# Kernel optimization log

Hardware: AMD Instinct MI355X
Metric: run time of the kernel (lower is better)

## Reference

```python
import jax, jax.numpy as jnp
import numpy as np

SAMPLE_SIZE = 8192
K = 8
N_SPLATS = 1_000_000
EPS = 1e-12  # keeps sqrt grad finite on zero-distance (duplicate) pairs


def setup_inputs() -> dict:
    key = jax.random.key(0)
    k1, k2, k3 = jax.random.split(key, 3)
    means = jax.random.normal(k1, (N_SPLATS, 3), dtype=jnp.float32)
    sh0 = jax.random.normal(k2, (N_SPLATS, 1, 3), dtype=jnp.float32)
    idx = jax.random.randint(k3, (SAMPLE_SIZE,), 0, N_SPLATS, dtype=jnp.int64)
    return {"means": means, "sh0": sh0, "idx": idx}


def reference(means, sh0, idx):
    sh0 = sh0.squeeze(1)                    # [N, 3]
    sm = means[idx]                         # [S, 3] sampled positions
    ss = sh0[idx]                           # [S, 3] sampled colors
    # pairwise euclidean distances (torch.cdist, p=2): [S, S]
    sq = jnp.sum(sm * sm, axis=-1)
    d2 = sq[:, None] + sq[None, :] - 2.0 * (sm @ sm.T)
    dist = jnp.sqrt(jnp.maximum(d2, EPS))
    # k+1 smallest per row; drop self (column 0)
    _, knn_idx = jax.lax.top_k(-dist, K + 1)           # [S, K+1]
    knn_idx = knn_idx[:, 1:]                           # [S, K]
    neighbors_sh0 = ss[knn_idx]                        # [S, K, 3]
    neighbor_dist = jnp.take_along_axis(dist, knn_idx, axis=1)[..., None]  # [S, K, 1]
    weight = jnp.exp(-neighbor_dist)
    diff = ss[:, None, :] - neighbors_sh0              # [S, K, 3]
    return jnp.mean(weight * diff * diff)
```

## Files before the change

### kernel.cpp

```cpp
#include <hip/hip_runtime.h>
#include <float.h>
#include <math.h>

#define NSAMPLE 8192
#define KSEL 9
#define KNN 8
#define BLK 256
#define EPS_F 1e-12f

#define ROWS_PB 8
#define PAIRS 4
#define SUBS 64
#define KPT (NSAMPLE / SUBS)
#define BNDK 32
#define BATCH 4
#define SLOTS 256
#define SLOTP 257
#define IDX_MASK 0x1FFFu
#define VAL_MASK 0xFFFFE000u
#define PROW 73
#define SROW 289
#define SCALE (1.0f / (float)(NSAMPLE * KNN * 3))

__device__ __forceinline__ unsigned umn(unsigned a, unsigned b) { return a < b ? a : b; }
__device__ __forceinline__ unsigned umx(unsigned a, unsigned b) { return a > b ? a : b; }

__device__ __forceinline__ void insert9(unsigned s[KSEL], unsigned x)
{
#pragma unroll
    for (int k = 0; k < KSEL - 1; ++k)
        s[k] = umx(s[k + 1], umn(x, s[k]));
    s[KSEL - 1] = umn(x, s[KSEL - 1]);
}

__device__ __forceinline__ unsigned pack_d2(float d2, int gidx)
{
    return (__float_as_uint(fmaxf(d2, 0.0f)) & VAL_MASK) | (unsigned)gidx;
}

__global__ __launch_bounds__(256) void gather_k(
    const float* __restrict__ means, const float* __restrict__ sh0,
    const int* __restrict__ idx,
    float4* __restrict__ sm4, float4* __restrict__ ss4)
{
    int i = blockIdx.x * 256 + threadIdx.x;
    if (i >= NSAMPLE) return;
    int id = idx[i];
    const float* m = means + 3 * id;
    const float* s = sh0 + 3 * id;
    float mx = m[0], my = m[1], mz = m[2];
    sm4[i] = make_float4(mx, my, mz, fmaf(mx, mx, fmaf(my, my, mz * mz)));
    ss4[i] = make_float4(s[0], s[1], s[2], 0.0f);
}

__global__ __launch_bounds__(BLK, 4) void main_k(
    const float4* __restrict__ sm4, const float4* __restrict__ ss4,
    float* __restrict__ out)
{
    __shared__ unsigned surv[ROWS_PB * SLOTP];
    __shared__ unsigned scratch[ROWS_PB * SROW];
    __shared__ unsigned bpart[ROWS_PB * SUBS];
    __shared__ unsigned partS[ROWS_PB * PROW];
    __shared__ unsigned scnt[ROWS_PB];
    __shared__ unsigned bnd[ROWS_PB];
    __shared__ float    red[ROWS_PB];

    const int t = threadIdx.x;
    const int sub = t & (SUBS - 1);
    const int pair = t >> 6;
    const int rowA = pair, rowB = pair + PAIRS;
    if (t < ROWS_PB) scnt[t] = 0u;

    const float4 pA = sm4[blockIdx.x * ROWS_PB + rowA];
    const float4 pB = sm4[blockIdx.x * ROWS_PB + rowB];
    const float aX = -2.0f * pA.x, aY = -2.0f * pA.y, aZ = -2.0f * pA.z, aW = pA.w;
    const float bX = -2.0f * pB.x, bY = -2.0f * pB.y, bZ = -2.0f * pB.z, bW = pB.w;

    {
        unsigned pmA = 0xFFFFFFFFu, pmB = 0xFFFFFFFFu;
#pragma unroll 8
        for (int k = 0; k < BNDK; ++k) {
            float4 q = sm4[k * SUBS + sub];
            float sA = aW + q.w, sB = bW + q.w;
            float dA = fmaf(aX, q.x, fmaf(aY, q.y, fmaf(aZ, q.z, sA)));
            float dB = fmaf(bX, q.x, fmaf(bY, q.y, fmaf(bZ, q.z, sB)));
            pmA = umn(pmA, pack_d2(dA, k * SUBS + sub));
            pmB = umn(pmB, pack_d2(dB, k * SUBS + sub));
        }
        bpart[rowA * SUBS + sub] = pmA;
        bpart[rowB * SUBS + sub] = pmB;
    }
    __syncthreads();
    if (t < ROWS_PB) {
        unsigned s[KSEL];
#pragma unroll
        for (int k = 0; k < KSEL; ++k) s[k] = 0xFFFFFFFFu;
#pragma unroll
        for (int e = 0; e < SUBS; ++e) insert9(s, bpart[t * SUBS + e]);
        bnd[t] = s[0];
    }
    __syncthreads();

    const float bfA = __uint_as_float(bnd[rowA] | IDX_MASK);
    const float bfB = __uint_as_float(bnd[rowB] | IDX_MASK);

    for (int k0 = 0; k0 < KPT; k0 += BATCH) {
        float4 qr[BATCH];
#pragma unroll
        for (int u = 0; u < BATCH; ++u)
            qr[u] = sm4[(k0 + u) * SUBS + sub];
#pragma unroll
        for (int u = 0; u < BATCH; ++u) {
            float sA = aW + qr[u].w, sB = bW + qr[u].w;
            float dA = fmaf(aX, qr[u].x, fmaf(aY, qr[u].y, fmaf(aZ, qr[u].z, sA)));
            float dB = fmaf(bX, qr[u].x, fmaf(bY, qr[u].y, fmaf(bZ, qr[u].z, sB)));
            bool cA = (dA <= bfA), cB = (dB <= bfB);
            if (__any(cA || cB)) {
                int ci = (k0 + u) * SUBS + sub;
                if (cA) {
                    unsigned pos = atomicAdd(&scnt[rowA], 1u);
                    if (pos < SLOTS) surv[rowA * SLOTP + pos] = pack_d2(dA, ci);
                }
                if (cB) {
                    unsigned pos = atomicAdd(&scnt[rowB], 1u);
                    if (pos < SLOTS) surv[rowB * SLOTP + pos] = pack_d2(dB, ci);
                }
            }
        }
    }
    __syncthreads();

    {
        const int r1 = t & (ROWS_PB - 1);
        const int g  = t >> 3;
        const unsigned n = umn(scnt[r1], SLOTS);
        unsigned s[KSEL];
#pragma unroll
        for (int k = 0; k < KSEL; ++k) s[k] = 0xFFFFFFFFu;
        for (unsigned k = g; k < n; k += 32)
            insert9(s, surv[r1 * SLOTP + k]);
#pragma unroll
        for (int k = 0; k < KSEL; ++k)
            scratch[r1 * SROW + g * KSEL + k] = s[k];
    }
    __syncthreads();

    if (t < ROWS_PB * 8) {
        const int r1 = t & (ROWS_PB - 1);
        const int mg = t >> 3;
        unsigned m[KSEL];
#pragma unroll
        for (int k = 0; k < KSEL; ++k) m[k] = 0xFFFFFFFFu;
#pragma unroll
        for (int e = 0; e < 4 * KSEL; ++e)
            insert9(m, scratch[r1 * SROW + (4 * mg) * KSEL + e]);
#pragma unroll
        for (int k = 0; k < KSEL; ++k)
            partS[r1 * PROW + mg * KSEL + k] = m[k];
    }
    __syncthreads();

    if (t < ROWS_PB) {
        unsigned m[KSEL];
#pragma unroll
        for (int k = 0; k < KSEL; ++k) m[k] = 0xFFFFFFFFu;
#pragma unroll
        for (int e = 0; e < 8 * KSEL; ++e)
            insert9(m, partS[t * PROW + e]);

        const int gr = blockIdx.x * ROWS_PB + t;
        float4 pm4 = sm4[gr];
        float4 ps4 = ss4[gr];
        float acc = 0.0f;
#pragma unroll
        for (int k = 0; k < KNN; ++k) {
            int j = (int)(m[k] & IDX_MASK);
            float4 qm = sm4[j];
            float dx = pm4.x - qm.x, dy = pm4.y - qm.y, dz = pm4.z - qm.z;
            float d2 = fmaf(dx, dx, fmaf(dy, dy, dz * dz));
            float d = sqrtf(fmaxf(d2, EPS_F));
            float w = expf(-d);
            float4 qs = ss4[j];
            float ax = ps4.x - qs.x, ay = ps4.y - qs.y, az = ps4.z - qs.z;
            acc += w * (ax * ax + ay * ay + az * az);
        }
        red[t] = acc;
    }
    __syncthreads();
    if (t == 0) {
        float ssum = 0.0f;
#pragma unroll
        for (int i = 0; i < ROWS_PB; ++i) ssum += red[i];
        atomicAdd(out, ssum * SCALE);
    }
}

extern "C" void kernel_launch(void* const* d_in, const int* in_sizes, int n_in,
                              void* d_out, int out_size, void* d_ws, size_t ws_size,
                              hipStream_t stream)
{
    const float* means = (const float*)d_in[0];
    const float* sh0   = (const float*)d_in[1];
    const int*   idxp  = (const int*)d_in[2];

    float4* sm4 = (float4*)d_ws;
    float4* ss4 = sm4 + NSAMPLE;

    gather_k<<<NSAMPLE / 256, 256, 0, stream>>>(means, sh0, idxp, sm4, ss4);
    main_k<<<NSAMPLE / ROWS_PB, BLK, 0, stream>>>(sm4, ss4, (float*)d_out);
}
```

Measured before the change: 112.3 us.

## Use 512-thread blocks with 4 rows per thread and candidate-range split across waves

Doubles the block to 512 threads. Each thread now handles 4 query rows over a quarter of the candidate range instead of 2 rows over the full range, so each loaded candidate is reused across more rows. The bound-estimation pass samples 2048 candidates with a hierarchical top-9 reduction instead of 2048 over one serial 64-way merge. The ballot-gated survivor insertion is now done per row. This raises register pressure (launch bounds of 8) and adds extra synchronised reduction stages before the main scan.

After: 104.9 us. 1.07x faster.

```diff
diff --git a/kernel.cpp b/kernel.cpp
--- a/kernel.cpp
+++ b/kernel.cpp
@@ -5,17 +5,18 @@
 #define NSAMPLE 8192
 #define KSEL 9
 #define KNN 8
-#define BLK 256
+#define BLK 512
 #define EPS_F 1e-12f
 
 #define ROWS_PB 8
-#define PAIRS 4
-#define SUBS 64
-#define KPT (NSAMPLE / SUBS)
-#define BNDK 32
+#define RPT 4
+#define LANES 64
+#define KQT 32
+#define BNDI 8
 #define BATCH 4
 #define SLOTS 256
-#define SLOTP 257
+#define SLOTP 260
+#define BP 264
 #define IDX_MASK 0x1FFFu
 #define VAL_MASK 0xFFFFE000u
 #define PROW 73
@@ -53,86 +54,133 @@
     ss4[i] = make_float4(s[0], s[1], s[2], 0.0f);
 }
 
-__global__ __launch_bounds__(BLK, 4) void main_k(
+__global__ __launch_bounds__(BLK, 8) void main_k(
     const float4* __restrict__ sm4, const float4* __restrict__ ss4,
     float* __restrict__ out)
 {
     __shared__ unsigned surv[ROWS_PB * SLOTP];
     __shared__ unsigned scratch[ROWS_PB * SROW];
-    __shared__ unsigned bpart[ROWS_PB * SUBS];
+    __shared__ unsigned bpart[ROWS_PB * BP];
     __shared__ unsigned partS[ROWS_PB * PROW];
     __shared__ unsigned scnt[ROWS_PB];
     __shared__ unsigned bnd[ROWS_PB];
     __shared__ float    red[ROWS_PB];
 
     const int t = threadIdx.x;
-    const int sub = t & (SUBS - 1);
-    const int pair = t >> 6;
-    const int rowA = pair, rowB = pair + PAIRS;
+    const int lane = t & (LANES - 1);
+    const int w = t >> 6;
+    const int rpar = w & 1;
+    const int quarter = w >> 1;
     if (t < ROWS_PB) scnt[t] = 0u;
 
-    const float4 pA = sm4[blockIdx.x * ROWS_PB + rowA];
-    const float4 pB = sm4[blockIdx.x * ROWS_PB + rowB];
-    const float aX = -2.0f * pA.x, aY = -2.0f * pA.y, aZ = -2.0f * pA.z, aW = pA.w;
-    const float bX = -2.0f * pB.x, bY = -2.0f * pB.y, bZ = -2.0f * pB.z, bW = pB.w;
+    float cX[RPT], cY[RPT], cZ[RPT], cW[RPT];
+#pragma unroll
+    for (int i = 0; i < RPT; ++i) {
+        float4 p = sm4[blockIdx.x * ROWS_PB + rpar + 2 * i];
+        cX[i] = -2.0f * p.x; cY[i] = -2.0f * p.y; cZ[i] = -2.0f * p.z;
+        cW[i] = p.w;
+    }
 
     {
-        unsigned pmA = 0xFFFFFFFFu, pmB = 0xFFFFFFFFu;
-#pragma unroll 8
-        for (int k = 0; k < BNDK; ++k) {
-            float4 q = sm4[k * SUBS + sub];
-            float sA = aW + q.w, sB = bW + q.w;
-            float dA = fmaf(aX, q.x, fmaf(aY, q.y, fmaf(aZ, q.z, sA)));
-            float dB = fmaf(bX, q.x, fmaf(bY, q.y, fmaf(bZ, q.z, sB)));
-            pmA = umn(pmA, pack_d2(dA, k * SUBS + sub));
-            pmB = umn(pmB, pack_d2(dB, k * SUBS + sub));
+        unsigned pm[RPT];
+#pragma unroll
+        for (int i = 0; i < RPT; ++i) pm[i] = 0xFFFFFFFFu;
+        const int b0 = quarter * (BNDI * LANES);
+#pragma unroll
+        for (int k = 0; k < BNDI; ++k) {
+            const int ci = b0 + k * LANES + lane;
+            float4 q = sm4[ci];
+#pragma unroll
+            for (int i = 0; i < RPT; ++i) {
+                float d2 = fmaf(cX[i], q.x,
+                           fmaf(cY[i], q.y, fmaf(cZ[i], q.z, cW[i] + q.w)));
+                pm[i] = umn(pm[i], pack_d2(d2, ci));
+            }
         }
-        bpart[rowA * SUBS + sub] = pmA;
-        bpart[rowB * SUBS + sub] = pmB;
+#pragma unroll
+        for (int i = 0; i < RPT; ++i)
+            bpart[(rpar + 2 * i) * BP + quarter * LANES + lane] = pm[i];
+    }
+    __syncthreads();
+
+    if (t < 256) {
+        const int r1 = t & (ROWS_PB - 1);
+        const int g = t >> 3;
+        unsigned s[KSEL];
+#pragma unroll
+        for (int k = 0; k < KSEL; ++k) s[k] = 0xFFFFFFFFu;
+#pragma unroll
+        for (int e = 0; e < 8; ++e)
+            insert9(s, bpart[r1 * BP + g * 8 + e]);
+#pragma unroll
+        for (int k = 0; k < KSEL; ++k)
+            scratch[r1 * SROW + g * KSEL + k] = s[k];
+    }
+    __syncthreads();
+    if (t < 64) {
+        const int r1 = t & (ROWS_PB - 1);
+        const int mg = t >> 3;
+        unsigned m[KSEL];
+#pragma unroll
+        for (int k = 0; k < KSEL; ++k) m[k] = 0xFFFFFFFFu;
+#pragma unroll
+        for (int e = 0; e < 4 * KSEL; ++e)
+            insert9(m, scratch[r1 * SROW + (4 * mg) * KSEL + e]);
+#pragma unroll
+        for (int k = 0; k < KSEL; ++k)
+            partS[r1 * PROW + mg * KSEL + k] = m[k];
     }
     __syncthreads();
     if (t < ROWS_PB) {
-        unsigned s[KSEL];
-#pragma unroll
-        for (int k = 0; k < KSEL; ++k) s[k] = 0xFFFFFFFFu;
-#pragma unroll
-        for (int e = 0; e < SUBS; ++e) insert9(s, bpart[t * SUBS + e]);
-        bnd[t] = s[0];
-    }
-    __syncthreads();
-
-    const float bfA = __uint_as_float(bnd[rowA] | IDX_MASK);
-    const float bfB = __uint_as_float(bnd[rowB] | IDX_MASK);
-
-    for (int k0 = 0; k0 < KPT; k0 += BATCH) {
+        unsigned m[KSEL];
+#pragma unroll
+        for (int k = 0; k < KSEL; ++k) m[k] = 0xFFFFFFFFu;
+#pragma unroll
+        for (int e = 0; e < 8 * KSEL; ++e)
+            insert9(m, partS[t * PROW + e]);
+        bnd[t] = m[0];
+    }
+    __syncthreads();
+
+    float bf[RPT];
+#pragma unroll
+    for (int i = 0; i < RPT; ++i)
+        bf[i] = __uint_as_float(bnd[rpar + 2 * i] | IDX_MASK);
+
+    const int s0 = quarter * (KQT * LANES);
+    for (int k0 = 0; k0 < KQT; k0 += BATCH) {
         float4 qr[BATCH];
 #pragma unroll
         for (int u = 0; u < BATCH; ++u)
-            qr[u] = sm4[(k0 + u) * SUBS + sub];
+            qr[u] = sm4[s0 + (k0 + u) * LANES + lane];
 #pragma unroll
         for (int u = 0; u < BATCH; ++u) {
-            float sA = aW + qr[u].w, sB = bW + qr[u].w;
-            float dA = fmaf(aX, qr[u].x, fmaf(aY, qr[u].y, fmaf(aZ, qr[u].z, sA)));
-            float dB = fmaf(bX, qr[u].x, fmaf(bY, qr[u].y, fmaf(bZ, qr[u].z, sB)));
-            bool cA = (dA <= bfA), cB = (dB <= bfB);
-            if (__any(cA || cB)) {
-                int ci = (k0 + u) * SUBS + sub;
-                if (cA) {
-                    unsigned pos = atomicAdd(&scnt[rowA], 1u);
-                    if (pos < SLOTS) surv[rowA * SLOTP + pos] = pack_d2(dA, ci);
-                }
-                if (cB) {
-                    unsigned pos = atomicAdd(&scnt[rowB], 1u);
-                    if (pos < SLOTS) surv[rowB * SLOTP + pos] = pack_d2(dB, ci);
+            const int ci = s0 + (k0 + u) * LANES + lane;
+            float d[RPT];
+#pragma unroll
+            for (int i = 0; i < RPT; ++i)
+                d[i] = fmaf(cX[i], qr[u].x,
+                       fmaf(cY[i], qr[u].y,
+                       fmaf(cZ[i], qr[u].z, cW[i] + qr[u].w)));
+#pragma unroll
+            for (int i = 0; i < RPT; ++i) {
+                bool c = (d[i] <= bf[i]);
+                if (__any(c)) {
+                    if (c) {
+                        const int r = rpar + 2 * i;
+                        unsigned pos = atomicAdd(&scnt[r], 1u);
+                        if (pos < SLOTS)
+                            surv[r * SLOTP + pos] = pack_d2(d[i], ci);
+                    }
                 }
             }
         }
     }
     __syncthreads();
 
-    {
-        const int r1 = t & (ROWS_PB - 1);
-        const int g  = t >> 3;
+    if (t < 256) {
+        const int r1 = t & (ROWS_PB - 1);
+        const int g = t >> 3;
         const unsigned n = umn(scnt[r1], SLOTS);
         unsigned s[KSEL];
 #pragma unroll
@@ -144,8 +192,7 @@
             scratch[r1 * SROW + g * KSEL + k] = s[k];
     }
     __syncthreads();
-
-    if (t < ROWS_PB * 8) {
+    if (t < 64) {
         const int r1 = t & (ROWS_PB - 1);
         const int mg = t >> 3;
         unsigned m[KSEL];
@@ -179,10 +226,10 @@
             float dx = pm4.x - qm.x, dy = pm4.y - qm.y, dz = pm4.z - qm.z;
             float d2 = fmaf(dx, dx, fmaf(dy, dy, dz * dz));
             float d = sqrtf(fmaxf(d2, EPS_F));
-            float w = expf(-d);
+            float wgt = expf(-d);
             float4 qs = ss4[j];
             float ax = ps4.x - qs.x, ay = ps4.y - qs.y, az = ps4.z - qs.z;
-            acc += w * (ax * ax + ay * ay + az * az);
+            acc += wgt * (ax * ax + ay * ay + az * az);
         }
         red[t] = acc;
     }
```
